# Optimization experiments

Hardware: AMD Instinct MI355X
Metric: run time of the kernel (lower is better)

## Reference

```python
import jax, jax.numpy as jnp
import numpy as np

H_DIM = 1024
N_HEADS = 16
HEAD_DIM = H_DIM // N_HEADS
MAX_POS = 2048   # RotaryEmbedding default max_position_embeddings
BASE = 10000.0
SCALING_FACTOR = 1.0


def rotate_half(x):
    # interleaved convention: cat([-x[..., 1::2], x[..., ::2]], -1)
    return jnp.concatenate([-x[..., 1::2], x[..., ::2]], axis=-1)


def rope_cos_sin(seq_len, dtype):
    # LlamaDynamicNTKScalingRotaryEmbedding._set_cos_sin_cache
    base = BASE
    if seq_len > MAX_POS:
        base = BASE * (SCALING_FACTOR * seq_len / MAX_POS - (SCALING_FACTOR - 1.0)) ** (HEAD_DIM / (HEAD_DIM - 2))
    inv_freq = 1.0 / (base ** (jnp.arange(0, HEAD_DIM, 2, dtype=jnp.float32) / HEAD_DIM))
    t = jnp.arange(seq_len, dtype=jnp.float32)
    freqs = jnp.einsum('i,j->ij', t, inv_freq)          # [S, D/2]
    emb = jnp.concatenate([freqs, freqs], axis=-1)       # [S, D]
    return emb.astype(dtype), jnp.cos(emb).astype(dtype), jnp.sin(emb).astype(dtype)


def setup_inputs() -> dict:
    key = jax.random.key(0)
    ks = jax.random.split(key, 5)
    B, S = 1, 4096
    scale_w = 0.02
    return {
        'hidden_states': jax.random.normal(ks[0], (B, S, H_DIM), dtype=jnp.float32),
        'Wq': jax.random.normal(ks[1], (H_DIM, H_DIM), dtype=jnp.float32) * scale_w,
        'Wk': jax.random.normal(ks[2], (H_DIM, H_DIM), dtype=jnp.float32) * scale_w,
        'Wv': jax.random.normal(ks[3], (H_DIM, H_DIM), dtype=jnp.float32) * scale_w,
        'Wo': jax.random.normal(ks[4], (H_DIM, H_DIM), dtype=jnp.float32) * scale_w,
    }


def reference(hidden_states, Wq, Wk, Wv, Wo):
    B, S, H = hidden_states.shape
    # projections (nn.Linear: x @ W.T)
    def proj(x, W):
        y = jnp.einsum('bsh,oh->bso', x, W)
        return y.reshape(B, S, N_HEADS, HEAD_DIM).transpose(0, 2, 1, 3)  # bhsd
    q = proj(hidden_states, Wq)
    k = proj(hidden_states, Wk)
    v = proj(hidden_states, Wv)

    _, cos, sin = rope_cos_sin(S, hidden_states.dtype)
    cos = cos[None, None, :, :]   # [1,1,S,D] (position_ids = arange(S)[None], unsqueeze(1))
    sin = sin[None, None, :, :]
    q = q * cos + rotate_half(q) * sin
    k = k * cos + rotate_half(k) * sin

    # NOTE: source DIVIDES by scale = head_dim**-0.5 (i.e. multiplies by sqrt(d))
    scale = HEAD_DIM ** (-0.5)
    attn = jnp.einsum('bhsd,bhtd->bhst', q, k) / scale
    attn = jax.nn.softmax(attn, axis=-1)
    out = jnp.einsum('bhst,bhtd->bhsd', attn, v)
    out = out.transpose(0, 2, 1, 3).reshape(B, S, H)
    return jnp.einsum('bsh,oh->bso', out, Wo)
```

## Files before the change

### kernel.cpp

```cpp
#include <hip/hip_runtime.h>
#include <cmath>
#include <cstdint>

#define S_LEN 4096
#define NH 16
#define HD 64

typedef _Float16 f16x8 __attribute__((ext_vector_type(8)));
typedef __attribute__((ext_vector_type(4))) float f32x4;
typedef __attribute__((ext_vector_type(16))) float f32x16;
typedef __attribute__((ext_vector_type(4))) unsigned short u16x4;
typedef __attribute__((ext_vector_type(4))) unsigned int u32x4;
typedef int i32x2 __attribute__((ext_vector_type(2)));
typedef __attribute__((ext_vector_type(4))) float f4;

__device__ __forceinline__ unsigned short f2h(float x) {
  union { _Float16 h; unsigned short u; } v; v.h = (_Float16)x; return v.u;
}
__device__ __forceinline__ float h2f(unsigned short u) {
  union { unsigned short u; _Float16 h; } v; v.u = u; return (float)v.h;
}
__device__ __forceinline__ float permx32(float v) {
  int idx = (((int)(threadIdx.x & 63)) ^ 32) << 2;
  return __int_as_float(__builtin_amdgcn_ds_bpermute(idx, __float_as_int(v)));
}
__device__ __forceinline__ float exp2a(float x) {
  float r; asm("v_exp_f32 %0, %1" : "=v"(r) : "v"(x)); return r;
}
__device__ __forceinline__ unsigned pkh(float a, float b) {
  unsigned r;
  asm("v_cvt_pkrtz_f16_f32 %0, %1, %2" : "=v"(r) : "v"(a), "v"(b));
  return r;
}
__device__ __forceinline__ float max3a(float a, float b, float c) {
  float r;
  asm("v_max3_f32 %0, %1, %2, %3" : "=v"(r) : "v"(a), "v"(b), "v"(c));
  return r;
}

#define GLL16(g, l) __builtin_amdgcn_global_load_lds( \
    (const __attribute__((address_space(1))) void*)(g), \
    (__attribute__((address_space(3))) void*)(l), 16, 0, 0)

#define PLANE_BYTES 524288
#define TILE_BYTES 8192

__global__ __launch_bounds__(256) void cvt_table_kernel(
    const float* __restrict__ hs, const float* __restrict__ wq,
    const float* __restrict__ wk, const float* __restrict__ wv,
    const float* __restrict__ wo,
    unsigned short* __restrict__ hs16,
    unsigned short* __restrict__ wq16, unsigned short* __restrict__ wk16,
    unsigned short* __restrict__ wv16, unsigned short* __restrict__ wo16,
    float* __restrict__ cosT, float* __restrict__ sinT, double base)
{
  if (blockIdx.x >= 4096) {
    int idx = (blockIdx.x - 4096) * 256 + threadIdx.x;
    if (idx < S_LEN * 32) {
      int t = idx >> 5, j = idx & 31;
      double invf = pow(base, -(double)j / 32.0);
      double f = fmod((double)t * invf, 6.283185307179586476925286766559);
      float ff = (float)f;
      cosT[idx] = cosf(ff);
      sinT[idx] = sinf(ff);
    }
    return;
  }
  const int HID4 = (S_LEN * 1024) / 4;
  const int W4   = (1024 * 1024) / 4;
  const int total = HID4 + 4 * W4;
  for (int i = blockIdx.x * 256 + threadIdx.x; i < total; i += 4096 * 256) {
    const float* s; unsigned short* d; int off;
    if (i < HID4) { s = hs; d = hs16; off = i; }
    else {
      int j = i - HID4; int w = j >> 18; off = j & (W4 - 1);
      s = (w == 0) ? wq : (w == 1) ? wk : (w == 2) ? wv : wo;
      d = (w == 0) ? wq16 : (w == 1) ? wk16 : (w == 2) ? wv16 : wo16;
    }
    f4 v = *(const f4*)(s + (size_t)off * 4);
    u16x4 r;
#pragma unroll
    for (int j = 0; j < 4; j++) r[j] = f2h(v[j]);
    *(u16x4*)(d + (size_t)off * 4) = r;
  }
}

__global__ __launch_bounds__(256) void gemm_f16(
    const unsigned short* __restrict__ A,
    const unsigned short* __restrict__ B0, const unsigned short* __restrict__ B1,
    const unsigned short* __restrict__ B2,
    void* O0, void* O1, void* O2, int M, int K, int fin)
{
  __shared__ unsigned short As[128 * 64];
  __shared__ unsigned short Bs[128 * 64];
  const int z = blockIdx.z;
  const unsigned short* B = (z == 0) ? B0 : (z == 1) ? B1 : B2;
  void* O = (z == 0) ? O0 : (z == 1) ? O1 : O2;
  const int m0 = blockIdx.y * 128, n0 = blockIdx.x * 128;
  const int tid = threadIdx.x, wid = tid >> 6, lane = tid & 63;
  const int lr = lane & 15, lk = (lane >> 4) * 8;
  const int wr = (wid >> 1) * 64, wc = (wid & 1) * 64;
  const int strow = lane >> 3;
  const int stcol = (lane & 7) * 8;

  f32x4 acc[4][4];
#pragma unroll
  for (int m = 0; m < 4; m++)
#pragma unroll
    for (int n = 0; n < 4; n++) acc[m][n] = (f32x4){0.f, 0.f, 0.f, 0.f};

  for (int kt = 0; kt < K; kt += 64) {
#pragma unroll
    for (int i = 0; i < 4; i++) {
      int c = wid * 4 + i;
      int row = c * 8 + strow;
      GLL16(A + (size_t)(m0 + row) * K + kt + stcol, &As[c * 512]);
      GLL16(B + (size_t)(n0 + row) * K + kt + stcol, &Bs[c * 512]);
    }
    __syncthreads();
    f16x8 af[4][2], bfr[4][2];
#pragma unroll
    for (int m = 0; m < 4; m++)
#pragma unroll
      for (int kk = 0; kk < 2; kk++)
        af[m][kk] = *(const f16x8*)&As[(wr + m * 16 + lr) * 64 + kk * 32 + lk];
#pragma unroll
    for (int n = 0; n < 4; n++)
#pragma unroll
      for (int kk = 0; kk < 2; kk++)
        bfr[n][kk] = *(const f16x8*)&Bs[(wc + n * 16 + lr) * 64 + kk * 32 + lk];
#pragma unroll
    for (int m = 0; m < 4; m++)
#pragma unroll
      for (int n = 0; n < 4; n++)
#pragma unroll
        for (int kk = 0; kk < 2; kk++)
          acc[m][n] = __builtin_amdgcn_mfma_f32_16x16x32_f16(
              af[m][kk], bfr[n][kk], acc[m][n], 0, 0, 0);
    __syncthreads();
  }

  const int rbase = m0 + wr + (lane >> 4) * 4;
  const int cbase = n0 + wc + lr;
  if (fin) {
    float* C = (float*)O;
#pragma unroll
    for (int m = 0; m < 4; m++)
#pragma unroll
      for (int n = 0; n < 4; n++)
#pragma unroll
        for (int j = 0; j < 4; j++) {
          int s = rbase + m * 16 + j;
          int o = cbase + n * 16;
          C[(size_t)s * 1024 + o] = acc[m][n][j];
        }
  } else if (z == 2) {
    char* base = (char*)O;
#pragma unroll
    for (int m = 0; m < 4; m++)
#pragma unroll
      for (int n = 0; n < 4; n++) {
        int s = rbase + m * 16;
        int o = cbase + n * 16;
        int hd = o >> 6, d = o & 63;
        size_t tb = (size_t)hd * PLANE_BYTES + (size_t)(s >> 6) * TILE_BYTES
                  + (size_t)d * 128;
        int cbyte = (2 * (s & 63)) ^ ((d & 7) << 4);
        u16x4 r;
#pragma unroll
        for (int j = 0; j < 4; j++) r[j] = f2h(acc[m][n][j]);
        *(u16x4*)(base + tb + cbyte) = r;
      }
  } else {
    unsigned short* C = (unsigned short*)O;
#pragma unroll
    for (int m = 0; m < 4; m++)
#pragma unroll
      for (int n = 0; n < 4; n++)
#pragma unroll
        for (int j = 0; j < 4; j++) {
          int s = rbase + m * 16 + j;
          int o = cbase + n * 16;
          C[((size_t)(o >> 6) * M + s) * HD + (o & 63)] = f2h(acc[m][n][j]);
        }
  }
}

__global__ __launch_bounds__(256) void rope_apply(
    const unsigned short* __restrict__ Qh, const unsigned short* __restrict__ Kh,
    unsigned short* __restrict__ Q16, char* __restrict__ Kt,
    const float* __restrict__ cosT, const float* __restrict__ sinT)
{
  int wid = threadIdx.x >> 6, lane = threadIdx.x & 63;
  int row = blockIdx.x * 4 + wid;
  int t = row & (S_LEN - 1);
  int head = row >> 12;
  int j = (lane < 32) ? lane : (lane - 32);
  float c = cosT[t * 32 + j], s = sinT[t * 32 + j];
  int partner = (lane < 32) ? (2 * lane + 1) : (2 * (lane - 32));
  float sgn = (lane < 32) ? -1.0f : 1.0f;
  float q = h2f(Qh[(size_t)row * HD + lane]);
  float k = h2f(Kh[(size_t)row * HD + lane]);
  float qo = __shfl(q, partner, 64);
  float ko = __shfl(k, partner, 64);
  float qr = (q * c + sgn * qo * s) * 11.541560327111707f;
  float kr = k * c + sgn * ko * s;
  Q16[(size_t)row * HD + lane] = f2h(qr);
  size_t kb = (size_t)head * PLANE_BYTES + (size_t)(t >> 6) * TILE_BYTES
            + (size_t)(t & 63) * 128 + ((2 * lane) ^ ((t & 7) << 4));
  *(unsigned short*)(Kt + kb) = f2h(kr);
}

__global__ __launch_bounds__(256, 4) void attn_kernel(
    const unsigned short* __restrict__ Q16, const char* __restrict__ Kt,
    const char* __restrict__ Vt,
    unsigned short* __restrict__ Opart, float* __restrict__ Ml)
{
  __shared__ char KL[2][TILE_BYTES];
  __shared__ char VL[2][TILE_BYTES];

  const int tid = threadIdx.x, wid = tid >> 6, lane = tid & 63;
  const int l5 = lane & 31, hi2 = lane >> 5;
  const int z = blockIdx.z;

  int id = blockIdx.x + 32 * blockIdx.y;
  int h  = (id & 7) + 8 * ((id >> 3) & 1);
  int bx = id >> 4;
  const int qw = bx * 128 + wid * 32;

  const size_t hoff = (size_t)h * PLANE_BYTES;
  const char* KtH = Kt + hoff;
  const char* VtH = Vt + hoff;

  const unsigned short* Qrow = Q16 + ((size_t)h * S_LEN + qw + l5) * HD;
  f16x8 qf[4];
#pragma unroll
  for (int ks = 0; ks < 4; ks++)
    qf[ks] = *(const f16x8*)&Qrow[ks * 16 + hi2 * 8];

  f32x16 o0 = (f32x16)0.0f, o1 = (f32x16)0.0f;
  float m_q = -__builtin_inff(), l_q = 0.f;

  const int T0 = z * 32;
  const int NT = 32;

#define STAGE(kt, b) do { \
    size_t tb = (size_t)(T0 + (kt)) * TILE_BYTES; \
    _Pragma("unroll") \
    for (int c = 0; c < 2; c++) { \
      int ub = c * 4096 + wid * 1024; \
      int go = ub + lane * 16; \
      GLL16(KtH + tb + go, &KL[b][ub]); \
      GLL16(VtH + tb + go, &VL[b][ub]); \
    } } while (0)

#define QKT(b) do { \
    s0 = (f32x16)0.0f; s1 = (f32x16)0.0f; \
    __builtin_amdgcn_s_setprio(1); \
    _Pragma("unroll") \
    for (int ks = 0; ks < 4; ks++) { \
      const int coff = (32 * ks + 16 * hi2) ^ ((l5 & 7) << 4); \
      f16x8 k0 = *(const f16x8*)(&KL[b][l5 * 128 + coff]); \
      f16x8 k1 = *(const f16x8*)(&KL[b][(32 + l5) * 128 + coff]); \
      s0 = __builtin_amdgcn_mfma_f32_32x32x16_f16(k0, qf[ks], s0, 0, 0, 0); \
      s1 = __builtin_amdgcn_mfma_f32_32x32x16_f16(k1, qf[ks], s1, 0, 0, 0); \
    } \
    __builtin_amdgcn_s_setprio(0); \
  } while (0)

  STAGE(0, 0);
  asm volatile("s_waitcnt vmcnt(0)" ::: "memory");
  __builtin_amdgcn_s_barrier();
  asm volatile("" ::: "memory");
  STAGE(1, 1);

  f32x16 s0, s1;
  QKT(0);

  for (int kt = 0; kt < NT; ++kt) {
    const int cur = kt & 1;

    float t0 = max3a(s0[0],  s0[1],  s0[2]);
    float t1 = max3a(s0[3],  s0[4],  s0[5]);
    float t2 = max3a(s0[6],  s0[7],  s0[8]);
    float t3 = max3a(s0[9],  s0[10], s0[11]);
    float t4 = max3a(s0[12], s0[13], s0[14]);
    float t5 = max3a(s0[15], s1[0],  s1[1]);
    float t6 = max3a(s1[2],  s1[3],  s1[4]);
    float t7 = max3a(s1[5],  s1[6],  s1[7]);
    float t8 = max3a(s1[8],  s1[9],  s1[10]);
    float t9 = max3a(s1[11], s1[12], s1[13]);
    float ta = fmaxf(s1[14], s1[15]);
    float u0 = max3a(t0, t1, t2);
    float u1 = max3a(t3, t4, t5);
    float u2 = max3a(t6, t7, t8);
    float u3 = fmaxf(t9, ta);
    float mx = fmaxf(max3a(u0, u1, u2), u3);
    mx = fmaxf(mx, permx32(mx));

    if (__any(mx > m_q + 11.0f)) {
      float mnew = fmaxf(m_q, mx);
      float alpha = exp2a(m_q - mnew);
      m_q = mnew;
      l_q *= alpha;
#pragma unroll
      for (int i = 0; i < 16; i++) { o0[i] *= alpha; o1[i] *= alpha; }
    }

    f16x8 pf[4];
    float g[4];
#pragma unroll
    for (int ks = 0; ks < 4; ks++) {
      f32x16 sv = (ks < 2) ? s0 : s1;
      const int base = (ks & 1) * 8;
      float e0 = exp2a(sv[base + 0] - m_q);
      float e1 = exp2a(sv[base + 1] - m_q);
      float e2 = exp2a(sv[base + 2] - m_q);
      float e3 = exp2a(sv[base + 3] - m_q);
      float e4 = exp2a(sv[base + 4] - m_q);
      float e5 = exp2a(sv[base + 5] - m_q);
      float e6 = exp2a(sv[base + 6] - m_q);
      float e7 = exp2a(sv[base + 7] - m_q);
      g[ks] = ((e0 + e1) + (e2 + e3)) + ((e4 + e5) + (e6 + e7));
      unsigned a0 = pkh(e0, e1);
      unsigned a1 = pkh(e2, e3);
      unsigned b0 = pkh(e4, e5);
      unsigned b1 = pkh(e6, e7);
      i32x2 r0 = __builtin_amdgcn_permlane32_swap((int)a0, (int)b0, false, false);
      i32x2 r1 = __builtin_amdgcn_permlane32_swap((int)a1, (int)b1, false, false);
      u32x4 w;
      w[0] = (unsigned)r0[0];
      w[1] = (unsigned)r1[0];
      w[2] = (unsigned)r0[1];
      w[3] = (unsigned)r1[1];
      union { u32x4 u; f16x8 f; } cv; cv.u = w;
      pf[ks] = cv.f;
    }
    float rs = (g[0] + g[1]) + (g[2] + g[3]);
    rs += permx32(rs);
    l_q += rs;

    if (kt + 1 < NT) {
      asm volatile("s_waitcnt vmcnt(0)" ::: "memory");
      __builtin_amdgcn_s_barrier();
      asm volatile("" ::: "memory");
      QKT(cur ^ 1);
    }

    __builtin_amdgcn_s_setprio(1);
#pragma unroll
    for (int ks = 0; ks < 4; ks++) {
      const int coff = (32 * ks + 16 * hi2) ^ ((l5 & 7) << 4);
      f16x8 v0 = *(const f16x8*)(&VL[cur][l5 * 128 + coff]);
      f16x8 v1 = *(const f16x8*)(&VL[cur][(32 + l5) * 128 + coff]);
      o0 = __builtin_amdgcn_mfma_f32_32x32x16_f16(v0, pf[ks], o0, 0, 0, 0);
      o1 = __builtin_amdgcn_mfma_f32_32x32x16_f16(v1, pf[ks], o1, 0, 0, 0);
    }
    __builtin_amdgcn_s_setprio(0);

    asm volatile("" ::: "memory");
    __builtin_amdgcn_s_barrier();
    asm volatile("" ::: "memory");
    if (kt + 2 < NT) STAGE(kt + 2, cur);
  }
#undef STAGE
#undef QKT

  const float inv = 1.0f / l_q;
  const int q = qw + l5;
  unsigned* orow = (unsigned*)(Opart + (((size_t)(z * NH + h)) * S_LEN + q) * HD);
#pragma unroll
  for (int k = 0; k < 8; k++) {
    const int d0 = 2 * (k & 1) + 8 * (k >> 1) + 4 * hi2;
    orow[d0 >> 1]        = pkh(o0[2 * k] * inv, o0[2 * k + 1] * inv);
    orow[(d0 + 32) >> 1] = pkh(o1[2 * k] * inv, o1[2 * k + 1] * inv);
  }
  if (hi2 == 0) {
    float2* mlp = (float2*)Ml + ((size_t)(z * NH + h)) * S_LEN + q;
    *mlp = make_float2(m_q, l_q);
  }
}

__global__ __launch_bounds__(256) void combine_kernel(
    const unsigned short* __restrict__ Opart, const float* __restrict__ Ml,
    unsigned short* __restrict__ Ab)
{
  const int NQ = S_LEN * 1024 / 4;
  for (int idx = blockIdx.x * 256 + threadIdx.x; idx < NQ;
       idx += gridDim.x * 256) {
    int e = idx * 4;
    int s = e >> 10;
    int col = e & 1023;
    int h = col >> 6, d = col & 63;
    const float2* mlb = (const float2*)Ml;
    float2 ml0 = mlb[(size_t)h * S_LEN + s];
    float2 ml1 = mlb[(size_t)(NH + h) * S_LEN + s];
    float mmax = fmaxf(ml0.x, ml1.x);
    float w0 = exp2f(ml0.x - mmax) * ml0.y;
    float w1 = exp2f(ml1.x - mmax) * ml1.y;
    float rden = 1.0f / (w0 + w1);
    float c0 = w0 * rden, c1 = w1 * rden;
    const unsigned short* p0 = Opart + ((size_t)h * S_LEN + s) * HD + d;
    const unsigned short* p1 = Opart + ((size_t)(NH + h) * S_LEN + s) * HD + d;
    u16x4 a = *(const u16x4*)p0;
    u16x4 b = *(const u16x4*)p1;
    u16x4 r;
#pragma unroll
    for (int j = 0; j < 4; j++)
      r[j] = f2h(c0 * h2f(a[j]) + c1 * h2f(b[j]));
    *(u16x4*)(Ab + e) = r;
  }
}

extern "C" void kernel_launch(void* const* d_in, const int* in_sizes, int n_in,
                              void* d_out, int out_size, void* d_ws, size_t ws_size,
                              hipStream_t stream)
{
  const float* hs = (const float*)d_in[0];
  const float* Wq = (const float*)d_in[1];
  const float* Wk = (const float*)d_in[2];
  const float* Wv = (const float*)d_in[3];
  const float* Wo = (const float*)d_in[4];

  char* ws = (char*)d_ws;
  const size_t HS = (size_t)S_LEN * 1024;
  const size_t WN = (size_t)1024 * 1024;
  size_t off = 0;
  unsigned short* hs16 = (unsigned short*)(ws + off); off += HS * 2;
  unsigned short* wq16 = (unsigned short*)(ws + off); off += WN * 2;
  unsigned short* wk16 = (unsigned short*)(ws + off); off += WN * 2;
  unsigned short* wv16 = (unsigned short*)(ws + off); off += WN * 2;
  unsigned short* wo16 = (unsigned short*)(ws + off); off += WN * 2;
  unsigned short* Qh16 = (unsigned short*)(ws + off); off += HS * 2;
  unsigned short* Kh16 = (unsigned short*)(ws + off); off += HS * 2;
  char* Kt_g = ws + off; off += (size_t)NH * PLANE_BYTES;
  char* VT_g = ws + off; off += (size_t)NH * PLANE_BYTES;
  unsigned short* Ab = (unsigned short*)(ws + off); off += HS * 2;
  float* Ml = (float*)(ws + off); off += (size_t)2 * NH * S_LEN * 8;
  float* cosT = (float*)(ws + off); off += (size_t)S_LEN * 32 * 4;
  float* sinT = (float*)(ws + off); off += (size_t)S_LEN * 32 * 4;
  unsigned short* Q16 = hs16;
  unsigned short* Opart = Qh16;

  double base = 10000.0 * pow((double)S_LEN / 2048.0, 64.0 / 62.0);

  cvt_table_kernel<<<4608, 256, 0, stream>>>(hs, Wq, Wk, Wv, Wo,
                                             hs16, wq16, wk16, wv16, wo16,
                                             cosT, sinT, base);

  gemm_f16<<<dim3(8, 32, 3), 256, 0, stream>>>(
      hs16, wq16, wk16, wv16, Qh16, Kh16, VT_g, S_LEN, 1024, 0);

  rope_apply<<<NH * S_LEN / 4, 256, 0, stream>>>(
      Qh16, Kh16, Q16, Kt_g, cosT, sinT);

  attn_kernel<<<dim3(32, 16, 2), 256, 0, stream>>>(
      Q16, Kt_g, VT_g, Opart, Ml);

  combine_kernel<<<2048, 256, 0, stream>>>(Opart, Ml, Ab);

  gemm_f16<<<dim3(8, 32, 1), 256, 0, stream>>>(
      Ab, wo16, wo16, wo16, d_out, d_out, d_out, S_LEN, 1024, 1);
}
```

Measured before the change: 200.4 us.

## Interleave PV MFMAs with softmax exp and use permlane32 swap for reductions

Moves the P·V MFMA loop into the softmax exponent loop so each 8-wide chunk of probabilities is consumed right away, and places it before the next tile's QK^T issue rather than after. The aim is to overlap exp/pack VALU work with matrix-core work and cut the registers held for the pf array. The cross-half max and sum reductions switch from ds_bpermute (an LDS-path op) to permlane32_swap. The setprio raise around PV is dropped, and the reordering changes how PV overlaps with the next QK^T, which could hurt the existing schedule.

New measurement: 195.5 us. -2.4%, faster.

```diff
diff --git a/kernel.cpp b/kernel.cpp
--- a/kernel.cpp
+++ b/kernel.cpp
@@ -20,10 +20,6 @@
 __device__ __forceinline__ float h2f(unsigned short u) {
   union { unsigned short u; _Float16 h; } v; v.u = u; return (float)v.h;
 }
-__device__ __forceinline__ float permx32(float v) {
-  int idx = (((int)(threadIdx.x & 63)) ^ 32) << 2;
-  return __int_as_float(__builtin_amdgcn_ds_bpermute(idx, __float_as_int(v)));
-}
 __device__ __forceinline__ float exp2a(float x) {
   float r; asm("v_exp_f32 %0, %1" : "=v"(r) : "v"(x)); return r;
 }
@@ -36,6 +32,11 @@
   float r;
   asm("v_max3_f32 %0, %1, %2, %3" : "=v"(r) : "v"(a), "v"(b), "v"(c));
   return r;
+}
+__device__ __forceinline__ float swapx32(float v, int hi2) {
+  i32x2 r = __builtin_amdgcn_permlane32_swap(__float_as_int(v), __float_as_int(v),
+                                             false, false);
+  return __int_as_float(hi2 ? r[0] : r[1]);
 }
 
 #define GLL16(g, l) __builtin_amdgcn_global_load_lds( \
@@ -296,7 +297,7 @@
     float u2 = max3a(t6, t7, t8);
     float u3 = fmaxf(t9, ta);
     float mx = fmaxf(max3a(u0, u1, u2), u3);
-    mx = fmaxf(mx, permx32(mx));
+    mx = fmaxf(mx, swapx32(mx, hi2));
 
     if (__any(mx > m_q + 11.0f)) {
       float mnew = fmaxf(m_q, mx);
@@ -307,21 +308,25 @@
       for (int i = 0; i < 16; i++) { o0[i] *= alpha; o1[i] *= alpha; }
     }
 
-    f16x8 pf[4];
-    float g[4];
+    float g0, g1, g2, g3;
 #pragma unroll
     for (int ks = 0; ks < 4; ks++) {
-      f32x16 sv = (ks < 2) ? s0 : s1;
       const int base = (ks & 1) * 8;
-      float e0 = exp2a(sv[base + 0] - m_q);
-      float e1 = exp2a(sv[base + 1] - m_q);
-      float e2 = exp2a(sv[base + 2] - m_q);
-      float e3 = exp2a(sv[base + 3] - m_q);
-      float e4 = exp2a(sv[base + 4] - m_q);
-      float e5 = exp2a(sv[base + 5] - m_q);
-      float e6 = exp2a(sv[base + 6] - m_q);
-      float e7 = exp2a(sv[base + 7] - m_q);
-      g[ks] = ((e0 + e1) + (e2 + e3)) + ((e4 + e5) + (e6 + e7));
+      float e0, e1, e2, e3, e4, e5, e6, e7;
+      if (ks < 2) {
+        e0 = exp2a(s0[base + 0] - m_q); e1 = exp2a(s0[base + 1] - m_q);
+        e2 = exp2a(s0[base + 2] - m_q); e3 = exp2a(s0[base + 3] - m_q);
+        e4 = exp2a(s0[base + 4] - m_q); e5 = exp2a(s0[base + 5] - m_q);
+        e6 = exp2a(s0[base + 6] - m_q); e7 = exp2a(s0[base + 7] - m_q);
+      } else {
+        e0 = exp2a(s1[base + 0] - m_q); e1 = exp2a(s1[base + 1] - m_q);
+        e2 = exp2a(s1[base + 2] - m_q); e3 = exp2a(s1[base + 3] - m_q);
+        e4 = exp2a(s1[base + 4] - m_q); e5 = exp2a(s1[base + 5] - m_q);
+        e6 = exp2a(s1[base + 6] - m_q); e7 = exp2a(s1[base + 7] - m_q);
+      }
+      float gs = ((e0 + e1) + (e2 + e3)) + ((e4 + e5) + (e6 + e7));
+      if (ks == 0) g0 = gs; else if (ks == 1) g1 = gs;
+      else if (ks == 2) g2 = gs; else g3 = gs;
       unsigned a0 = pkh(e0, e1);
       unsigned a1 = pkh(e2, e3);
       unsigned b0 = pkh(e4, e5);
@@ -334,10 +339,14 @@
       w[2] = (unsigned)r0[1];
       w[3] = (unsigned)r1[1];
       union { u32x4 u; f16x8 f; } cv; cv.u = w;
-      pf[ks] = cv.f;
-    }
-    float rs = (g[0] + g[1]) + (g[2] + g[3]);
-    rs += permx32(rs);
+      const int coff = (32 * ks + 16 * hi2) ^ ((l5 & 7) << 4);
+      f16x8 v0 = *(const f16x8*)(&VL[cur][l5 * 128 + coff]);
+      f16x8 v1 = *(const f16x8*)(&VL[cur][(32 + l5) * 128 + coff]);
+      o0 = __builtin_amdgcn_mfma_f32_32x32x16_f16(v0, cv.f, o0, 0, 0, 0);
+      o1 = __builtin_amdgcn_mfma_f32_32x32x16_f16(v1, cv.f, o1, 0, 0, 0);
+    }
+    float rs = (g0 + g1) + (g2 + g3);
+    rs += swapx32(rs, hi2);
     l_q += rs;
 
     if (kt + 1 < NT) {
@@ -346,17 +355,6 @@
       asm volatile("" ::: "memory");
       QKT(cur ^ 1);
     }
-
-    __builtin_amdgcn_s_setprio(1);
-#pragma unroll
-    for (int ks = 0; ks < 4; ks++) {
-      const int coff = (32 * ks + 16 * hi2) ^ ((l5 & 7) << 4);
-      f16x8 v0 = *(const f16x8*)(&VL[cur][l5 * 128 + coff]);
-      f16x8 v1 = *(const f16x8*)(&VL[cur][(32 + l5) * 128 + coff]);
-      o0 = __builtin_amdgcn_mfma_f32_32x32x16_f16(v0, pf[ks], o0, 0, 0, 0);
-      o1 = __builtin_amdgcn_mfma_f32_32x32x16_f16(v1, pf[ks], o1, 0, 0, 0);
-    }
-    __builtin_amdgcn_s_setprio(0);
 
     asm volatile("" ::: "memory");
     __builtin_amdgcn_s_barrier();
```
